# Optimization experiments

Measured on AMD Instinct MI355X. Metric: run time of the kernel, lower is better.

## Reference

```python
import jax, jax.numpy as jnp
import numpy as np

B, H, S, D = 8, 8, 2048, 64
NEG = -1e9


def setup_inputs() -> dict:
    key = jax.random.key(0)
    k1, k2, k3, k4 = jax.random.split(key, 4)
    query = jax.random.normal(k1, (B, H, S, D), dtype=jnp.float32)
    kk = jax.random.normal(k2, (B, H, S, D), dtype=jnp.float32)
    value = jax.random.normal(k3, (B, H, S, D), dtype=jnp.float32)
    mask = jax.random.randint(k4, (B, S, S), 0, 2, dtype=jnp.int32)
    return {"query": query, "key": kk, "value": value, "mask": mask}


def reference(query, key, value, mask):
    dk = key.shape[-1]
    # scores: [B,H,S,S] = (q/sqrt(dk)) @ k^T
    scores = jnp.einsum('bhqd,bhkd->bhqk', query / np.sqrt(dk), key)
    # mask broadcast over heads: [B,1,S,S]
    scores = jnp.where(mask[:, None, :, :] == 0, NEG, scores)
    attn = jax.nn.softmax(scores.astype(jnp.float32), axis=-1).astype(query.dtype)
    # dropout is identity in eval/deterministic reference
    return jnp.einsum('bhqk,bhkd->bhqd', attn, value)
```

## Files before the change

kernel.cpp:

```cpp
#include <hip/hip_runtime.h>
#include <hip/hip_bf16.h>
#include <stdint.h>


#define B_ 8
#define H_ 8
#define S_ 2048
#define D_ 64
#define QT 128
#define KT 64
#define NT (S_ / KT)
#define LOG2E 1.44269504088896340736f
#define QSCALE (0.125f * LOG2E)
#define THR 11.0f

typedef __bf16 bf16;
typedef bf16 bf16x8 __attribute__((ext_vector_type(8)));
typedef float f32x4 __attribute__((ext_vector_type(4)));
typedef unsigned short ushort8_t __attribute__((ext_vector_type(8)));
typedef unsigned long long u64;

#if __has_builtin(__builtin_amdgcn_exp2f)
#define EXP2(x) __builtin_amdgcn_exp2f(x)
#else
#define EXP2(x) exp2f(x)
#endif

static __device__ __forceinline__ unsigned short bfb(float f) {
    bf16 h = (bf16)f;
    return __builtin_bit_cast(unsigned short, h);
}
static __device__ __forceinline__ int phi_inv(int c) {
    return ((c >> 5) & 1) * 32 + ((c >> 2) & 1) * 16 + ((c >> 4) & 1) * 8 +
           ((c >> 3) & 1) * 4 + (c & 3);
}
static __device__ __forceinline__ void gload16(const unsigned short* g, unsigned short* l) {
    __builtin_amdgcn_global_load_lds(
        (const __attribute__((address_space(1))) unsigned int*)g,
        (__attribute__((address_space(3))) unsigned int*)l, 16, 0, 0);
}

__global__ __launch_bounds__(256) void mask_bits_kernel(const int* __restrict__ M,
                                                        u64* __restrict__ W) {
    const int ln = threadIdx.x & 63;
    const int w0 = blockIdx.x * 32 + (threadIdx.x >> 6) * 8;
#pragma unroll
    for (int j = 0; j < 8; ++j) {
        const int v = M[(long)(w0 + j) * 64 + ln];
        const u64 bal = __ballot(v != 0);
        if (ln == 0) W[w0 + j] = bal;
    }
}

__global__ __launch_bounds__(256) void prep_kv(const float* __restrict__ K,
                                               const float* __restrict__ V,
                                               unsigned short* __restrict__ Ko,
                                               unsigned short* __restrict__ Vo) {
    __shared__ float Vl[64][65];
    const int tid = threadIdx.x;
    const int t = blockIdx.x & (NT - 1);
    const int bh = blockIdx.x >> 5;
    const float* Kg = K + ((long)bh * S_ + t * 64) * D_;
    const float* Vg = V + ((long)bh * S_ + t * 64) * D_;
    unsigned short* Kout = Ko + ((long)bh * S_ + t * 64) * D_;
    unsigned short* Vout = Vo + (long)bh * D_ * S_ + t * 64;

    {
        const int kv = tid >> 2, d0 = (tid & 3) * 16;
#pragma unroll
        for (int half = 0; half < 2; ++half) {
            const float4 f0 = *(const float4*)(Kg + kv * D_ + d0 + half * 8);
            const float4 f1 = *(const float4*)(Kg + kv * D_ + d0 + half * 8 + 4);
            ushort8_t u;
            u[0] = bfb(f0.x); u[1] = bfb(f0.y); u[2] = bfb(f0.z); u[3] = bfb(f0.w);
            u[4] = bfb(f1.x); u[5] = bfb(f1.y); u[6] = bfb(f1.z); u[7] = bfb(f1.w);
            *(ushort8_t*)(Kout + kv * D_ + d0 + half * 8) = u;
        }
    }
    {
#pragma unroll
        for (int i = 0; i < 4; ++i) {
            const int kv = i * 16 + (tid >> 4);
            const int d4 = (tid & 15) * 4;
            const float4 f = *(const float4*)(Vg + kv * D_ + d4);
            Vl[kv][d4 + 0] = f.x; Vl[kv][d4 + 1] = f.y;
            Vl[kv][d4 + 2] = f.z; Vl[kv][d4 + 3] = f.w;
        }
    }
    __syncthreads();
    {
#pragma unroll
        for (int j = 0; j < 4; ++j) {
            const int chunk = j * 256 + tid;
            const int d = chunk >> 4, q4 = chunk & 15;
            ushort4 w;
            w.x = bfb(Vl[phi_inv(q4 * 4 + 0)][d]);
            w.y = bfb(Vl[phi_inv(q4 * 4 + 1)][d]);
            w.z = bfb(Vl[phi_inv(q4 * 4 + 2)][d]);
            w.w = bfb(Vl[phi_inv(q4 * 4 + 3)][d]);
            *(ushort4*)(Vout + (long)d * S_ + q4 * 4) = w;
        }
    }
}

template <int MODE>
__global__ __launch_bounds__(512, 4) void attn_fwd(
    const float* __restrict__ Q, const float* __restrict__ K,
    const float* __restrict__ V, const int* __restrict__ M,
    const u64* __restrict__ W, const unsigned short* __restrict__ Kp,
    const unsigned short* __restrict__ Vp, float* __restrict__ O)
{
    __shared__ __attribute__((aligned(16))) unsigned short Ks[2][KT * D_];
    __shared__ __attribute__((aligned(16))) unsigned short Vt[2][D_ * KT];

    const int tid = threadIdx.x;
    const int wv = tid >> 6, ln = tid & 63;
    const int col = ln & 15, grp = ln >> 4;

    int bid = blockIdx.x;
    bid = (bid & 7) * 128 + (bid >> 3);
    const int qt = bid & 15;
    const int h = (bid >> 4) & 7;
    const int b = bid >> 7;
    const int q0 = qt * QT;
    const int qw = q0 + wv * 16;

    const float* Qg = Q + ((long)((b * H_ + h) * S_) + qw + col) * D_;
    bf16x8 qf[2];
#pragma unroll
    for (int c = 0; c < 2; ++c) {
        const float4 a0 = *(const float4*)(Qg + c * 32 + grp * 8);
        const float4 a1 = *(const float4*)(Qg + c * 32 + grp * 8 + 4);
        qf[c][0] = (bf16)(a0.x * QSCALE); qf[c][1] = (bf16)(a0.y * QSCALE);
        qf[c][2] = (bf16)(a0.z * QSCALE); qf[c][3] = (bf16)(a0.w * QSCALE);
        qf[c][4] = (bf16)(a1.x * QSCALE); qf[c][5] = (bf16)(a1.y * QSCALE);
        qf[c][6] = (bf16)(a1.z * QSCALE); qf[c][7] = (bf16)(a1.w * QSCALE);
    }

    f32x4 oacc[4];
#pragma unroll
    for (int i = 0; i < 4; ++i) oacc[i] = (f32x4){0.f, 0.f, 0.f, 0.f};
    float mrun = -3.0e38f, lrun = 0.f;

    const u64* Wg = (MODE >= 1) ? (W + ((long)b * S_ + qw + col) * (S_ / 64)) : nullptr;
    const int* Mg = (MODE == 0) ? (M + ((long)b * S_ + qw + col) * S_) : nullptr;
    const unsigned short* Kbh = Kp + (long)(b * H_ + h) * S_ * D_;
    const unsigned short* Vbh = Vp + (long)(b * H_ + h) * D_ * S_;
    const float* Kf = K + (long)(b * H_ + h) * S_ * D_;
    const float* Vf = V + (long)(b * H_ + h) * S_ * D_;

    const int rl = ln >> 3;
    const int c8 = (ln & 7) ^ rl;
    const int krow = wv * 8 + rl;

    float4 ka[2];
    float va[8];
    const int vd = ln, kg0 = wv;

    auto STAGE_ISSUE = [&](int kv0, int buf) {
        gload16(Kbh + (long)(kv0 + krow) * D_ + c8 * 8, &Ks[buf][0] + wv * 512);
        gload16(Vbh + (long)krow * S_ + kv0 + c8 * 8, &Vt[buf][0] + wv * 512);
    };
    auto LOADT = [&](int kv0) {
#pragma unroll
        for (int i = 0; i < 2; ++i) {
            const int idx4 = i * 512 + tid;
            const int row = idx4 >> 4, c4 = idx4 & 15;
            ka[i] = *(const float4*)(Kf + (long)(kv0 + row) * D_ + c4 * 4);
        }
#pragma unroll
        for (int i = 0; i < 2; ++i) {
            const int kg = kg0 + i * 8;
            const int kvn = phi_inv(kg * 4);
#pragma unroll
            for (int j = 0; j < 4; ++j)
                va[i * 4 + j] = Vf[(long)(kv0 + kvn + j) * D_ + vd];
        }
    };
    auto WRITET = [&](int buf) {
#pragma unroll
        for (int i = 0; i < 2; ++i) {
            const int idx4 = i * 512 + tid;
            const int row = idx4 >> 4, c4 = idx4 & 15;
            const int byte = (row * 128 + c4 * 8) ^ ((row & 7) << 4);
            ushort4 w;
            w.x = bfb(ka[i].x); w.y = bfb(ka[i].y);
            w.z = bfb(ka[i].z); w.w = bfb(ka[i].w);
            *(ushort4*)((char*)Ks[buf] + byte) = w;
        }
#pragma unroll
        for (int i = 0; i < 2; ++i) {
            const int kg = kg0 + i * 8;
            const int byte = (vd * 128 + kg * 8) ^ ((vd & 7) << 4);
            ushort4 w;
            w.x = bfb(va[i * 4 + 0]); w.y = bfb(va[i * 4 + 1]);
            w.z = bfb(va[i * 4 + 2]); w.w = bfb(va[i * 4 + 3]);
            *(ushort4*)((char*)Vt[buf] + byte) = w;
        }
    };

    auto STEP = [&](int t, const unsigned short* Kc, const unsigned short* Vc) {
        f32x4 sc[4];
#pragma unroll
        for (int blk = 0; blk < 4; ++blk) {
            sc[blk] = (f32x4){0.f, 0.f, 0.f, 0.f};
#pragma unroll
            for (int c = 0; c < 2; ++c) {
                const int row = blk * 16 + col;
                const int byte = (row * 128 + c * 64 + grp * 16) ^ ((row & 7) << 4);
                const bf16x8 kf = *(const bf16x8*)((const char*)Kc + byte);
                sc[blk] = __builtin_amdgcn_mfma_f32_16x16x32_bf16(kf, qf[c], sc[blk], 0, 0, 0);
            }
        }
        float p[4][4];
        float rm = -3.0e38f;
        if (MODE >= 1) {
            const u64 mw = Wg[t];
#pragma unroll
            for (int blk = 0; blk < 4; ++blk)
#pragma unroll
                for (int r = 0; r < 4; ++r) {
                    const float s = ((mw >> (blk * 16 + grp * 4 + r)) & 1ull) ? sc[blk][r] : -1e9f;
                    p[blk][r] = s;
                    rm = fmaxf(rm, s);
                }
        } else {
#pragma unroll
            for (int blk = 0; blk < 4; ++blk)
#pragma unroll
                for (int r = 0; r < 4; ++r) {
                    const int mv = Mg[t * KT + blk * 16 + grp * 4 + r];
                    const float s = mv ? sc[blk][r] : -1e9f;
                    p[blk][r] = s;
                    rm = fmaxf(rm, s);
                }
        }
        rm = fmaxf(rm, __shfl_xor(rm, 16));
        rm = fmaxf(rm, __shfl_xor(rm, 32));
        if (__any(rm - mrun > THR)) {
            const float mn = fmaxf(mrun, rm);
            const float al = EXP2(mrun - mn);
            mrun = mn;
            lrun *= al;
#pragma unroll
            for (int r = 0; r < 4; ++r) {
                const float ar = __shfl(al, grp * 20 + r);
#pragma unroll
                for (int db = 0; db < 4; ++db) oacc[db][r] *= ar;
            }
        }
        float rs = 0.f;
#pragma unroll
        for (int blk = 0; blk < 4; ++blk)
#pragma unroll
            for (int r = 0; r < 4; ++r) {
                const float e = EXP2(p[blk][r] - mrun);
                p[blk][r] = e;
                rs += e;
            }
        rs += __shfl_xor(rs, 16);
        rs += __shfl_xor(rs, 32);
        lrun += rs;
        bf16x8 pf[2];
#pragma unroll
        for (int c = 0; c < 2; ++c)
#pragma unroll
            for (int j = 0; j < 8; ++j)
                pf[c][j] = (bf16)p[2 * c + (j >> 2)][j & 3];
#pragma unroll
        for (int c = 0; c < 2; ++c)
#pragma unroll
            for (int db = 0; db < 4; ++db) {
                const int vrow = db * 16 + col;
                const int byte = (vrow * 128 + c * 64 + grp * 16) ^ ((vrow & 7) << 4);
                const bf16x8 vf = *(const bf16x8*)((const char*)Vc + byte);
                oacc[db] = __builtin_amdgcn_mfma_f32_16x16x32_bf16(pf[c], vf, oacc[db], 0, 0, 0);
            }
    };

    if (MODE == 2) {
        STAGE_ISSUE(0, 0);
    } else {
        LOADT(0);
        WRITET(0);
    }
    __syncthreads();

#pragma unroll 1
    for (int t = 0; t < NT; ++t) {
        const int cur = t & 1;
        if (t + 1 < NT) {
            if (MODE == 2) STAGE_ISSUE((t + 1) * KT, cur ^ 1);
            else LOADT((t + 1) * KT);
        }
        STEP(t, Ks[cur], Vt[cur]);
        if (MODE < 2 && t + 1 < NT) WRITET(cur ^ 1);
        __syncthreads();
    }

    float* Og = O + ((long)((b * H_ + h) * S_) + qw) * D_;
#pragma unroll
    for (int r = 0; r < 4; ++r) {
        const float lr = __shfl(lrun, grp * 20 + r);
        const float inv = 1.0f / lr;
#pragma unroll
        for (int db = 0; db < 4; ++db)
            Og[(grp * 4 + r) * D_ + db * 16 + col] = oacc[db][r] * inv;
    }
}

extern "C" void kernel_launch(void* const* d_in, const int* in_sizes, int n_in,
                              void* d_out, int out_size, void* d_ws, size_t ws_size,
                              hipStream_t stream) {
    (void)in_sizes; (void)n_in; (void)out_size;
    const float* Q = (const float*)d_in[0];
    const float* K = (const float*)d_in[1];
    const float* V = (const float*)d_in[2];
    const int*   M = (const int*)d_in[3];
    float* O = (float*)d_out;

    const size_t szW = (size_t)B_ * S_ * (S_ / 64) * sizeof(u64);
    const size_t szK = (size_t)B_ * H_ * S_ * D_ * 2;
    const int grid = B_ * H_ * (S_ / QT);

    if (ws_size >= szW + 2 * szK) {
        u64* W = (u64*)d_ws;
        unsigned short* Kp = (unsigned short*)((char*)d_ws + szW);
        unsigned short* Vp = (unsigned short*)((char*)d_ws + szW + szK);
        const int nwords = B_ * S_ * (S_ / 64);
        mask_bits_kernel<<<nwords / 32, 256, 0, stream>>>(M, W);
        prep_kv<<<B_ * H_ * NT, 256, 0, stream>>>(K, V, Kp, Vp);
        attn_fwd<2><<<grid, 512, 0, stream>>>(Q, K, V, M, W, Kp, Vp, O);
    } else if (ws_size >= szW) {
        u64* W = (u64*)d_ws;
        const int nwords = B_ * S_ * (S_ / 64);
        mask_bits_kernel<<<nwords / 32, 256, 0, stream>>>(M, W);
        attn_fwd<1><<<grid, 512, 0, stream>>>(Q, K, V, M, W, nullptr, nullptr, O);
    } else {
        attn_fwd<0><<<grid, 512, 0, stream>>>(Q, K, V, M, nullptr, nullptr, nullptr, O);
    }
}
```

Before: 188.8 us.

## Fuse prep kernels, compute row sums via MFMA, add setprio and unroll KV loop

Merges the mask-bitpack and K/V bf16 conversion kernels into one launch, which removes one kernel launch and its gap. Inside attention, the softmax row sum now comes from extra MFMAs against a ones vector instead of scalar adds and cross-lane shuffles. It also splits the 64-bit mask word into 32-bit halves, raises wave priority around MFMA sections, and unrolls the KV loop by two so buffer indices are constant. The row sum is now taken from bf16-rounded probabilities, a small numeric change, and NT must stay even for the two-step loop.

```diff
diff --git a/kernel.cpp b/kernel.cpp
--- a/kernel.cpp
+++ b/kernel.cpp
@@ -40,31 +40,32 @@
         (__attribute__((address_space(3))) unsigned int*)l, 16, 0, 0);
 }
 
-__global__ __launch_bounds__(256) void mask_bits_kernel(const int* __restrict__ M,
-                                                        u64* __restrict__ W) {
-    const int ln = threadIdx.x & 63;
-    const int w0 = blockIdx.x * 32 + (threadIdx.x >> 6) * 8;
-#pragma unroll
-    for (int j = 0; j < 8; ++j) {
-        const int v = M[(long)(w0 + j) * 64 + ln];
-        const u64 bal = __ballot(v != 0);
-        if (ln == 0) W[w0 + j] = bal;
-    }
-}
-
-__global__ __launch_bounds__(256) void prep_kv(const float* __restrict__ K,
-                                               const float* __restrict__ V,
-                                               unsigned short* __restrict__ Ko,
-                                               unsigned short* __restrict__ Vo) {
+#define KV_BLOCKS (B_ * H_ * NT)
+
+__global__ __launch_bounds__(256) void prep_fused(
+    const float* __restrict__ K, const float* __restrict__ V,
+    unsigned short* __restrict__ Ko, unsigned short* __restrict__ Vo,
+    const int* __restrict__ M, u64* __restrict__ W) {
+    const int tid = threadIdx.x;
+    if (blockIdx.x >= KV_BLOCKS) {
+        const int ln = tid & 63;
+        const int w0 = (blockIdx.x - KV_BLOCKS) * 32 + (tid >> 6) * 8;
+#pragma unroll
+        for (int j = 0; j < 8; ++j) {
+            const int v = M[(long)(w0 + j) * 64 + ln];
+            const u64 bal = __ballot(v != 0);
+            if (ln == 0) W[w0 + j] = bal;
+        }
+        return;
+    }
+    if (Ko == nullptr) return;
     __shared__ float Vl[64][65];
-    const int tid = threadIdx.x;
     const int t = blockIdx.x & (NT - 1);
     const int bh = blockIdx.x >> 5;
     const float* Kg = K + ((long)bh * S_ + t * 64) * D_;
     const float* Vg = V + ((long)bh * S_ + t * 64) * D_;
     unsigned short* Kout = Ko + ((long)bh * S_ + t * 64) * D_;
     unsigned short* Vout = Vo + (long)bh * D_ * S_ + t * 64;
-
     {
         const int kv = tid >> 2, d0 = (tid & 3) * 16;
 #pragma unroll
@@ -122,8 +123,7 @@
     const int qt = bid & 15;
     const int h = (bid >> 4) & 7;
     const int b = bid >> 7;
-    const int q0 = qt * QT;
-    const int qw = q0 + wv * 16;
+    const int qw = qt * QT + wv * 16;
 
     const float* Qg = Q + ((long)((b * H_ + h) * S_) + qw + col) * D_;
     bf16x8 qf[2];
@@ -136,11 +136,15 @@
         qf[c][4] = (bf16)(a1.x * QSCALE); qf[c][5] = (bf16)(a1.y * QSCALE);
         qf[c][6] = (bf16)(a1.z * QSCALE); qf[c][7] = (bf16)(a1.w * QSCALE);
     }
+    bf16x8 onesf;
+#pragma unroll
+    for (int j = 0; j < 8; ++j) onesf[j] = (bf16)1.0f;
 
     f32x4 oacc[4];
 #pragma unroll
     for (int i = 0; i < 4; ++i) oacc[i] = (f32x4){0.f, 0.f, 0.f, 0.f};
-    float mrun = -3.0e38f, lrun = 0.f;
+    f32x4 accs = (f32x4){0.f, 0.f, 0.f, 0.f};
+    float mrun = -3.0e38f;
 
     const u64* Wg = (MODE >= 1) ? (W + ((long)b * S_ + qw + col) * (S_ / 64)) : nullptr;
     const int* Mg = (MODE == 0) ? (M + ((long)b * S_ + qw + col) * S_) : nullptr;
@@ -201,6 +205,7 @@
 
     auto STEP = [&](int t, const unsigned short* Kc, const unsigned short* Vc) {
         f32x4 sc[4];
+        __builtin_amdgcn_s_setprio(1);
 #pragma unroll
         for (int blk = 0; blk < 4; ++blk) {
             sc[blk] = (f32x4){0.f, 0.f, 0.f, 0.f};
@@ -212,18 +217,23 @@
                 sc[blk] = __builtin_amdgcn_mfma_f32_16x16x32_bf16(kf, qf[c], sc[blk], 0, 0, 0);
             }
         }
+        __builtin_amdgcn_s_setprio(0);
         float p[4][4];
         float rm = -3.0e38f;
         if (MODE >= 1) {
-            const u64 mw = Wg[t];
-#pragma unroll
-            for (int blk = 0; blk < 4; ++blk)
+            const u64 mws = Wg[t] >> (grp * 4);
+            const unsigned mlo = (unsigned)mws, mhi = (unsigned)(mws >> 32);
+#pragma unroll
+            for (int blk = 0; blk < 4; ++blk) {
+                const unsigned w32 = (blk < 2) ? mlo : mhi;
 #pragma unroll
                 for (int r = 0; r < 4; ++r) {
-                    const float s = ((mw >> (blk * 16 + grp * 4 + r)) & 1ull) ? sc[blk][r] : -1e9f;
+                    const int bit = (blk & 1) * 16 + r;
+                    const float s = ((w32 >> bit) & 1u) ? sc[blk][r] : -1e9f;
                     p[blk][r] = s;
                     rm = fmaxf(rm, s);
                 }
+            }
         } else {
 #pragma unroll
             for (int blk = 0; blk < 4; ++blk)
@@ -241,32 +251,23 @@
             const float mn = fmaxf(mrun, rm);
             const float al = EXP2(mrun - mn);
             mrun = mn;
-            lrun *= al;
 #pragma unroll
             for (int r = 0; r < 4; ++r) {
                 const float ar = __shfl(al, grp * 20 + r);
+                accs[r] *= ar;
 #pragma unroll
                 for (int db = 0; db < 4; ++db) oacc[db][r] *= ar;
             }
         }
-        float rs = 0.f;
-#pragma unroll
-        for (int blk = 0; blk < 4; ++blk)
-#pragma unroll
-            for (int r = 0; r < 4; ++r) {
-                const float e = EXP2(p[blk][r] - mrun);
-                p[blk][r] = e;
-                rs += e;
-            }
-        rs += __shfl_xor(rs, 16);
-        rs += __shfl_xor(rs, 32);
-        lrun += rs;
         bf16x8 pf[2];
 #pragma unroll
         for (int c = 0; c < 2; ++c)
 #pragma unroll
             for (int j = 0; j < 8; ++j)
-                pf[c][j] = (bf16)p[2 * c + (j >> 2)][j & 3];
+                pf[c][j] = (bf16)EXP2(p[2 * c + (j >> 2)][j & 3] - mrun);
+        __builtin_amdgcn_s_setprio(1);
+        accs = __builtin_amdgcn_mfma_f32_16x16x32_bf16(pf[0], onesf, accs, 0, 0, 0);
+        accs = __builtin_amdgcn_mfma_f32_16x16x32_bf16(pf[1], onesf, accs, 0, 0, 0);
 #pragma unroll
         for (int c = 0; c < 2; ++c)
 #pragma unroll
@@ -276,6 +277,7 @@
                 const bf16x8 vf = *(const bf16x8*)((const char*)Vc + byte);
                 oacc[db] = __builtin_amdgcn_mfma_f32_16x16x32_bf16(pf[c], vf, oacc[db], 0, 0, 0);
             }
+        __builtin_amdgcn_s_setprio(0);
     };
 
     if (MODE == 2) {
@@ -287,22 +289,27 @@
     __syncthreads();
 
 #pragma unroll 1
-    for (int t = 0; t < NT; ++t) {
-        const int cur = t & 1;
+    for (int t = 0; t < NT; t += 2) {
         if (t + 1 < NT) {
-            if (MODE == 2) STAGE_ISSUE((t + 1) * KT, cur ^ 1);
+            if (MODE == 2) STAGE_ISSUE((t + 1) * KT, 1);
             else LOADT((t + 1) * KT);
         }
-        STEP(t, Ks[cur], Vt[cur]);
-        if (MODE < 2 && t + 1 < NT) WRITET(cur ^ 1);
+        STEP(t, Ks[0], Vt[0]);
+        if (MODE < 2 && t + 1 < NT) WRITET(1);
         __syncthreads();
+        if (t + 2 < NT) {
+            if (MODE == 2) STAGE_ISSUE((t + 2) * KT, 0);
+            else LOADT((t + 2) * KT);
+        }
+        STEP(t + 1, Ks[1], Vt[1]);
+        if (MODE < 2 && t + 2 < NT) WRITET(0);
+        __syncthreads();
     }
 
     float* Og = O + ((long)((b * H_ + h) * S_) + qw) * D_;
 #pragma unroll
     for (int r = 0; r < 4; ++r) {
-        const float lr = __shfl(lrun, grp * 20 + r);
-        const float inv = 1.0f / lr;
+        const float inv = 1.0f / accs[r];
 #pragma unroll
         for (int db = 0; db < 4; ++db)
             Og[(grp * 4 + r) * D_ + db * 16 + col] = oacc[db][r] * inv;
@@ -322,19 +329,17 @@
     const size_t szW = (size_t)B_ * S_ * (S_ / 64) * sizeof(u64);
     const size_t szK = (size_t)B_ * H_ * S_ * D_ * 2;
     const int grid = B_ * H_ * (S_ / QT);
+    const int nmaskblk = (B_ * S_ * (S_ / 64)) / 32;
 
     if (ws_size >= szW + 2 * szK) {
         u64* W = (u64*)d_ws;
         unsigned short* Kp = (unsigned short*)((char*)d_ws + szW);
         unsigned short* Vp = (unsigned short*)((char*)d_ws + szW + szK);
-        const int nwords = B_ * S_ * (S_ / 64);
-        mask_bits_kernel<<<nwords / 32, 256, 0, stream>>>(M, W);
-        prep_kv<<<B_ * H_ * NT, 256, 0, stream>>>(K, V, Kp, Vp);
+        prep_fused<<<KV_BLOCKS + nmaskblk, 256, 0, stream>>>(K, V, Kp, Vp, M, W);
         attn_fwd<2><<<grid, 512, 0, stream>>>(Q, K, V, M, W, Kp, Vp, O);
     } else if (ws_size >= szW) {
         u64* W = (u64*)d_ws;
-        const int nwords = B_ * S_ * (S_ / 64);
-        mask_bits_kernel<<<nwords / 32, 256, 0, stream>>>(M, W);
+        prep_fused<<<KV_BLOCKS + nmaskblk, 256, 0, stream>>>(K, V, nullptr, nullptr, M, W);
         attn_fwd<1><<<grid, 512, 0, stream>>>(Q, K, V, M, W, nullptr, nullptr, O);
     } else {
         attn_fwd<0><<<grid, 512, 0, stream>>>(Q, K, V, M, nullptr, nullptr, nullptr, O);
```

Measured after the change: 172.2 us. -8.8%, faster.
